# Performance work log

Measured on AMD Instinct MI355X. Metric: run time of the kernel, lower is better.

The kernel has to match this reference:

```python
import jax, jax.numpy as jnp
import numpy as np

S = 4096
DMODEL = 1024
DK = 128

def setup_inputs() -> dict:
    key = jax.random.key(0)
    ks = jax.random.split(key, 7)
    X = jax.random.normal(ks[0], (S, DMODEL), dtype=jnp.float32)
    # nn.Linear(dmodel, dk): weight [dk, dmodel], bias [dk]
    sc = 1.0 / np.sqrt(DMODEL)
    Wq = jax.random.uniform(ks[1], (DK, DMODEL), jnp.float32, -sc, sc)
    bq = jax.random.uniform(ks[2], (DK,), jnp.float32, -sc, sc)
    Wk = jax.random.uniform(ks[3], (DK, DMODEL), jnp.float32, -sc, sc)
    bk = jax.random.uniform(ks[4], (DK,), jnp.float32, -sc, sc)
    Wv = jax.random.uniform(ks[5], (DK, DMODEL), jnp.float32, -sc, sc)
    bv = jax.random.uniform(ks[6], (DK,), jnp.float32, -sc, sc)
    return {"X": X, "Wq": Wq, "bq": bq, "Wk": Wk, "bk": bk, "Wv": Wv, "bv": bv}

def reference(X, Wq, bq, Wk, bk, Wv, bv):
    # QKV projections: [S, dk]
    Q = X @ Wq.T + bq
    K = X @ Wk.T + bk
    V = X @ Wv.T + bv
    scale = 1.0 / jnp.sqrt(jnp.asarray(DK, X.dtype))
    scores = (Q @ K.T) * scale  # [S, S]
    s = X.shape[0]
    causal = jnp.tril(jnp.ones((s, s), dtype=bool))  # True = keep
    scores = jnp.where(causal, scores, -jnp.inf)
    A = jax.nn.softmax(scores, axis=-1)  # dropout p=0 -> identity
    return A @ V  # [S, dk]
```

## Files before the change

### kernel.cpp

```cpp
#include <hip/hip_runtime.h>
#include <hip/hip_bf16.h>

#define S 4096
#define DMODEL 1024
#define DK 128

typedef __attribute__((ext_vector_type(8))) short  short8;
typedef __attribute__((ext_vector_type(4))) float  f32x4;

__device__ __forceinline__ unsigned short f2bf(float f) {
    return __builtin_bit_cast(unsigned short, __float2bfloat16(f));
}

__device__ __forceinline__ short8 cvt8(float4 a, float4 b) {
    short8 v;
    v[0] = (short)f2bf(a.x); v[1] = (short)f2bf(a.y);
    v[2] = (short)f2bf(a.z); v[3] = (short)f2bf(a.w);
    v[4] = (short)f2bf(b.x); v[5] = (short)f2bf(b.y);
    v[6] = (short)f2bf(b.z); v[7] = (short)f2bf(b.w);
    return v;
}

__global__ __launch_bounds__(256) void cvt_kernel(
    const float* __restrict__ X,
    const float* __restrict__ Wq, const float* __restrict__ Wk,
    const float* __restrict__ Wv,
    unsigned short* __restrict__ Xb, unsigned short* __restrict__ Wb)
{
    const int i = blockIdx.x * 256 + threadIdx.x;
    const float* __restrict__ src;
    unsigned short* __restrict__ dst;
    size_t off;
    if (i < 524288) {
        src = X; dst = Xb; off = (size_t)i * 8;
    } else {
        const int j   = i - 524288;
        const int sel = j >> 14, jj = j & 16383;
        src = sel == 0 ? Wq : sel == 1 ? Wk : Wv;
        dst = Wb + (size_t)sel * DK * DMODEL;
        off = (size_t)jj * 8;
    }
    const float4 a = *(const float4*)(src + off);
    const float4 b = *(const float4*)(src + off + 4);
    *(short8*)(dst + off) = cvt8(a, b);
}

__global__ __launch_bounds__(128) void proj_gemm(
    const unsigned short* __restrict__ Xb, const unsigned short* __restrict__ Wb,
    const float* __restrict__ bq, const float* __restrict__ bk,
    const float* __restrict__ bv,
    unsigned short* __restrict__ Qb, unsigned short* __restrict__ Kb,
    unsigned short* __restrict__ Vb)
{
    const int sel = blockIdx.y;
    const float* __restrict__ bias = sel == 0 ? bq : sel == 1 ? bk : bv;
    unsigned short* __restrict__ Out = sel == 0 ? Qb : sel == 1 ? Kb : Vb;
    const unsigned short* __restrict__ wbase = Wb + (size_t)sel * DK * DMODEL;

    const int tid = threadIdx.x, w = tid >> 6, lane = tid & 63;
    const int li = lane & 15, gl = lane >> 4;
    const int r0 = blockIdx.x * 16;
    const int n0 = w * 64;

    f32x4 acc[4];
    #pragma unroll
    for (int j = 0; j < 4; ++j)
        #pragma unroll
        for (int r = 0; r < 4; ++r) acc[j][r] = 0.f;

    const unsigned short* ap = &Xb[(size_t)(r0 + li) * DMODEL + 8 * gl];
    const unsigned short* bp0 = &wbase[(size_t)(n0 + li) * DMODEL + 8 * gl];
    const unsigned short* bp1 = bp0 + (size_t)16 * DMODEL;
    const unsigned short* bp2 = bp0 + (size_t)32 * DMODEL;
    const unsigned short* bp3 = bp0 + (size_t)48 * DMODEL;

    #pragma unroll 4
    for (int k0 = 0; k0 < DMODEL; k0 += 32) {
        const short8 a  = *(const short8*)(ap + k0);
        const short8 b0 = *(const short8*)(bp0 + k0);
        const short8 b1 = *(const short8*)(bp1 + k0);
        const short8 b2 = *(const short8*)(bp2 + k0);
        const short8 b3 = *(const short8*)(bp3 + k0);
        acc[0] = __builtin_amdgcn_mfma_f32_16x16x32_bf16(a, b0, acc[0], 0, 0, 0);
        acc[1] = __builtin_amdgcn_mfma_f32_16x16x32_bf16(a, b1, acc[1], 0, 0, 0);
        acc[2] = __builtin_amdgcn_mfma_f32_16x16x32_bf16(a, b2, acc[2], 0, 0, 0);
        acc[3] = __builtin_amdgcn_mfma_f32_16x16x32_bf16(a, b3, acc[3], 0, 0, 0);
    }

    #pragma unroll
    for (int j = 0; j < 4; ++j)
        #pragma unroll
        for (int r = 0; r < 4; ++r) {
            const int row = r0 + 4 * gl + r;
            const int col = n0 + 16 * j + li;
            Out[(size_t)row * DK + col] = f2bf(acc[j][r] + bias[col]);
        }
}

__global__ __launch_bounds__(256) void transpose_v(
    const unsigned short* __restrict__ Vb, unsigned short* __restrict__ Vt)
{
    __shared__ unsigned short tile[64][72];
    const int s0 = blockIdx.x * 64, d0 = blockIdx.y * 64;
    const int t = threadIdx.x;
    const int r = t >> 2, cc = (t & 3) * 16;

    const short8* src = (const short8*)&Vb[(size_t)(s0 + r) * DK + d0 + cc];
    const short8 a = src[0], b = src[1];
    #pragma unroll
    for (int i = 0; i < 8; ++i) {
        tile[r][cc + i]     = (unsigned short)a[i];
        tile[r][cc + 8 + i] = (unsigned short)b[i];
    }
    __syncthreads();

    short8 o0, o1;
    #pragma unroll
    for (int i = 0; i < 8; ++i) {
        o0[i] = (short)tile[cc + i][r];
        o1[i] = (short)tile[cc + 8 + i][r];
    }
    short8* dst = (short8*)&Vt[(size_t)(d0 + r) * S + s0 + cc];
    dst[0] = o0; dst[1] = o1;
}

__global__ __launch_bounds__(64) void attn_mfma(
    const unsigned short* __restrict__ Qb,
    const unsigned short* __restrict__ Kb,
    const unsigned short* __restrict__ Vt,
    float* __restrict__ OP, float* __restrict__ ML)
{
    const int b = blockIdx.x;
    int g = 0;
    while (4 * (g + 1) * (g + 2) <= b) ++g;
    const int off = b - 4 * g * (g + 1);
    const int t   = 8 * g + off / (g + 1);
    const int c   = off % (g + 1);
    const int kstart = c * 256;
    const int kend   = min((c + 1) * 256, 32 * t + 32);

    const int lane = threadIdx.x, li = lane & 15, gl = lane >> 4;

    __shared__ unsigned short Pl[32][40];

    short8 aq[2][4];
    #pragma unroll
    for (int qs = 0; qs < 2; ++qs)
        #pragma unroll
        for (int s = 0; s < 4; ++s)
            aq[qs][s] = *(const short8*)
                &Qb[(size_t)(32 * t + 16 * qs + li) * DK + 32 * s + 8 * gl];

    f32x4 accv[2][8];
    #pragma unroll
    for (int qs = 0; qs < 2; ++qs)
        #pragma unroll
        for (int n = 0; n < 8; ++n)
            #pragma unroll
            for (int r = 0; r < 4; ++r) accv[qs][n][r] = 0.f;

    float mrow[2][4], lrow[2][4];
    #pragma unroll
    for (int qs = 0; qs < 2; ++qs)
        #pragma unroll
        for (int r = 0; r < 4; ++r) { mrow[qs][r] = -1e30f; lrow[qs][r] = 0.f; }

    const float scale = 0.08838834764831845f;

    short8 bkc[2][4], bkn[2][4];
    #pragma unroll
    for (int kt = 0; kt < 2; ++kt)
        #pragma unroll
        for (int s = 0; s < 4; ++s)
            bkc[kt][s] = *(const short8*)
                &Kb[(size_t)(kstart + 16 * kt + li) * DK + 32 * s + 8 * gl];

    for (int kb = kstart; kb < kend; kb += 32) {
        short8 bv[8];
        #pragma unroll
        for (int n = 0; n < 8; ++n)
            bv[n] = *(const short8*)&Vt[(size_t)(16 * n + li) * S + kb + 8 * gl];

        f32x4 sc[2][2];
        #pragma unroll
        for (int qs = 0; qs < 2; ++qs)
            #pragma unroll
            for (int kt = 0; kt < 2; ++kt)
                #pragma unroll
                for (int r = 0; r < 4; ++r) sc[qs][kt][r] = 0.f;
        __builtin_amdgcn_s_setprio(1);
        #pragma unroll
        for (int qs = 0; qs < 2; ++qs)
            #pragma unroll
            for (int kt = 0; kt < 2; ++kt)
                #pragma unroll
                for (int s = 0; s < 4; ++s)
                    sc[qs][kt] = __builtin_amdgcn_mfma_f32_16x16x32_bf16(
                        aq[qs][s], bkc[kt][s], sc[qs][kt], 0, 0, 0);
        __builtin_amdgcn_s_setprio(0);

        const int kn = (kb + 32 < kend) ? kb + 32 : kb;
        #pragma unroll
        for (int kt = 0; kt < 2; ++kt)
            #pragma unroll
            for (int s = 0; s < 4; ++s)
                bkn[kt][s] = *(const short8*)
                    &Kb[(size_t)(kn + 16 * kt + li) * DK + 32 * s + 8 * gl];

        #pragma unroll
        for (int qs = 0; qs < 2; ++qs)
            #pragma unroll
            for (int kt = 0; kt < 2; ++kt)
                #pragma unroll
                for (int r = 0; r < 4; ++r) {
                    const int key = kb + 16 * kt + li;
                    const int q   = 32 * t + 16 * qs + 4 * gl + r;
                    sc[qs][kt][r] = (key > q) ? -1e30f : sc[qs][kt][r] * scale;
                }

        float tm[2][4];
        #pragma unroll
        for (int qs = 0; qs < 2; ++qs)
            #pragma unroll
            for (int r = 0; r < 4; ++r) {
                float v = fmaxf(sc[qs][0][r], sc[qs][1][r]);
                v = fmaxf(v, __shfl_xor(v, 1));
                v = fmaxf(v, __shfl_xor(v, 2));
                v = fmaxf(v, __shfl_xor(v, 4));
                v = fmaxf(v, __shfl_xor(v, 8));
                tm[qs][r] = v;
            }

        int need = 0;
        #pragma unroll
        for (int qs = 0; qs < 2; ++qs)
            #pragma unroll
            for (int r = 0; r < 4; ++r)
                need |= (tm[qs][r] > mrow[qs][r] + 6.f) ? 1 : 0;
        if (__any(need)) {
            #pragma unroll
            for (int qs = 0; qs < 2; ++qs)
                #pragma unroll
                for (int r = 0; r < 4; ++r) {
                    const float mnew = fmaxf(mrow[qs][r], tm[qs][r]);
                    const float corr = __expf(mrow[qs][r] - mnew);
                    lrow[qs][r] *= corr;
                    mrow[qs][r] = mnew;
                    #pragma unroll
                    for (int n = 0; n < 8; ++n) accv[qs][n][r] *= corr;
                }
        }

        #pragma unroll
        for (int qs = 0; qs < 2; ++qs)
            #pragma unroll
            for (int r = 0; r < 4; ++r) {
                const float p0 = __expf(sc[qs][0][r] - mrow[qs][r]);
                const float p1 = __expf(sc[qs][1][r] - mrow[qs][r]);
                sc[qs][0][r] = p0; sc[qs][1][r] = p1;
                float ps = p0 + p1;
                ps += __shfl_xor(ps, 1);
                ps += __shfl_xor(ps, 2);
                ps += __shfl_xor(ps, 4);
                ps += __shfl_xor(ps, 8);
                lrow[qs][r] += ps;
            }

        #pragma unroll
        for (int qs = 0; qs < 2; ++qs)
            #pragma unroll
            for (int kt = 0; kt < 2; ++kt)
                #pragma unroll
                for (int r = 0; r < 4; ++r)
                    Pl[16 * qs + 4 * gl + r][16 * kt + li] = f2bf(sc[qs][kt][r]);
        __syncthreads();
        const short8 pa0 = *(const short8*)&Pl[li][8 * gl];
        const short8 pa1 = *(const short8*)&Pl[16 + li][8 * gl];
        __syncthreads();

        __builtin_amdgcn_s_setprio(1);
        #pragma unroll
        for (int n = 0; n < 8; ++n) {
            accv[0][n] = __builtin_amdgcn_mfma_f32_16x16x32_bf16(pa0, bv[n], accv[0][n], 0, 0, 0);
            accv[1][n] = __builtin_amdgcn_mfma_f32_16x16x32_bf16(pa1, bv[n], accv[1][n], 0, 0, 0);
        }
        __builtin_amdgcn_s_setprio(0);

        #pragma unroll
        for (int kt = 0; kt < 2; ++kt)
            #pragma unroll
            for (int s = 0; s < 4; ++s) bkc[kt][s] = bkn[kt][s];
    }

    #pragma unroll
    for (int qs = 0; qs < 2; ++qs)
        #pragma unroll
        for (int n = 0; n < 8; ++n)
            #pragma unroll
            for (int r = 0; r < 4; ++r)
                OP[((size_t)b * 32 + 16 * qs + 4 * gl + r) * DK + 16 * n + li]
                    = accv[qs][n][r];
    if (li == 0) {
        #pragma unroll
        for (int qs = 0; qs < 2; ++qs)
            #pragma unroll
            for (int r = 0; r < 4; ++r) {
                ML[((size_t)b * 32 + 16 * qs + 4 * gl + r) * 2 + 0] = mrow[qs][r];
                ML[((size_t)b * 32 + 16 * qs + 4 * gl + r) * 2 + 1] = lrow[qs][r];
            }
    }
}

__global__ __launch_bounds__(DK) void merge_kernel(
    const float* __restrict__ OP, const float* __restrict__ ML,
    float* __restrict__ out)
{
    const int row = blockIdx.x, dv = threadIdx.x;
    const int t  = row >> 5, rl = row & 31;
    const int g  = t >> 3;
    const int base = 4 * g * (g + 1) + (t & 7) * (g + 1);

    float M = -1e30f;
    for (int c = 0; c <= g; ++c)
        M = fmaxf(M, ML[((size_t)(base + c) * 32 + rl) * 2]);
    float L = 0.f, o = 0.f;
    for (int c = 0; c <= g; ++c) {
        const float mc = ML[((size_t)(base + c) * 32 + rl) * 2 + 0];
        const float lc = ML[((size_t)(base + c) * 32 + rl) * 2 + 1];
        const float wgt = __expf(mc - M);
        L += lc * wgt;
        o += wgt * OP[((size_t)(base + c) * 32 + rl) * DK + dv];
    }
    out[(size_t)row * DK + dv] = o / L;
}

extern "C" void kernel_launch(void* const* d_in, const int* in_sizes, int n_in,
                              void* d_out, int out_size, void* d_ws, size_t ws_size,
                              hipStream_t stream)
{
    (void)in_sizes; (void)n_in; (void)out_size; (void)ws_size;
    const float* X  = (const float*)d_in[0];
    const float* Wq = (const float*)d_in[1];
    const float* bq = (const float*)d_in[2];
    const float* Wk = (const float*)d_in[3];
    const float* bk = (const float*)d_in[4];
    const float* Wv = (const float*)d_in[5];
    const float* bv = (const float*)d_in[6];
    float* out = (float*)d_out;

    unsigned short* Wb = (unsigned short*)d_ws;
    unsigned short* Qb = Wb + (size_t)3 * DK * DMODEL;
    unsigned short* Kb = Qb + (size_t)S * DK;
    unsigned short* Vb = Kb + (size_t)S * DK;
    unsigned short* Vt = Vb + (size_t)S * DK;
    unsigned short* Xb = Vt + (size_t)S * DK;
    float* OP = (float*)Xb;
    float* ML = OP + (size_t)1088 * 32 * DK;

    cvt_kernel<<<2240, 256, 0, stream>>>(X, Wq, Wk, Wv, Xb, Wb);
    proj_gemm<<<dim3(S / 16, 3), 128, 0, stream>>>(
        Xb, Wb, bq, bk, bv, Qb, Kb, Vb);
    transpose_v<<<dim3(S / 64, DK / 64), 256, 0, stream>>>(Vb, Vt);
    attn_mfma<<<1088, 64, 0, stream>>>(Qb, Kb, Vt, OP, ML);
    merge_kernel<<<S, DK, 0, stream>>>(OP, ML, out);
}
```

Baseline: 149.9 us.

## Fuse V transpose into projection, split-K finer, swap MFMA operands for per-lane softmax

The projection GEMM now writes V directly in transposed layout, so the separate transpose kernel goes away. Attention work is split into 128-key chunks instead of 256, giving 2112 blocks, and the blocks are launched in reverse order so the largest ones start first. The score MFMA has its operands swapped so each lane owns one query row, which reduces the softmax max/sum reductions to two cross-lane shuffles and lets P be written to LDS as vectors. The __syncthreads calls around the single-wave LDS exchange are removed. The finer split produces more partial results for the merge kernel to combine and write out.

After: 152.3 us. Within noise of the previous version (+1.6%).

```diff
diff --git a/kernel.cpp b/kernel.cpp
--- a/kernel.cpp
+++ b/kernel.cpp
@@ -4,9 +4,11 @@
 #define S 4096
 #define DMODEL 1024
 #define DK 128
+#define NB_ATTN 2112
 
 typedef __attribute__((ext_vector_type(8))) short  short8;
 typedef __attribute__((ext_vector_type(4))) float  f32x4;
+typedef __attribute__((ext_vector_type(4))) unsigned short u16x4;
 
 __device__ __forceinline__ unsigned short f2bf(float f) {
     return __builtin_bit_cast(unsigned short, __float2bfloat16(f));
@@ -50,11 +52,10 @@
     const float* __restrict__ bq, const float* __restrict__ bk,
     const float* __restrict__ bv,
     unsigned short* __restrict__ Qb, unsigned short* __restrict__ Kb,
-    unsigned short* __restrict__ Vb)
+    unsigned short* __restrict__ Vt)
 {
     const int sel = blockIdx.y;
     const float* __restrict__ bias = sel == 0 ? bq : sel == 1 ? bk : bv;
-    unsigned short* __restrict__ Out = sel == 0 ? Qb : sel == 1 ? Kb : Vb;
     const unsigned short* __restrict__ wbase = Wb + (size_t)sel * DK * DMODEL;
 
     const int tid = threadIdx.x, w = tid >> 6, lane = tid & 63;
@@ -68,7 +69,7 @@
         #pragma unroll
         for (int r = 0; r < 4; ++r) acc[j][r] = 0.f;
 
-    const unsigned short* ap = &Xb[(size_t)(r0 + li) * DMODEL + 8 * gl];
+    const unsigned short* ap  = &Xb[(size_t)(r0 + li) * DMODEL + 8 * gl];
     const unsigned short* bp0 = &wbase[(size_t)(n0 + li) * DMODEL + 8 * gl];
     const unsigned short* bp1 = bp0 + (size_t)16 * DMODEL;
     const unsigned short* bp2 = bp0 + (size_t)32 * DMODEL;
@@ -87,41 +88,27 @@
         acc[3] = __builtin_amdgcn_mfma_f32_16x16x32_bf16(a, b3, acc[3], 0, 0, 0);
     }
 
-    #pragma unroll
-    for (int j = 0; j < 4; ++j)
-        #pragma unroll
-        for (int r = 0; r < 4; ++r) {
-            const int row = r0 + 4 * gl + r;
+    if (sel < 2) {
+        unsigned short* __restrict__ Out = sel == 0 ? Qb : Kb;
+        #pragma unroll
+        for (int j = 0; j < 4; ++j)
+            #pragma unroll
+            for (int r = 0; r < 4; ++r) {
+                const int row = r0 + 4 * gl + r;
+                const int col = n0 + 16 * j + li;
+                Out[(size_t)row * DK + col] = f2bf(acc[j][r] + bias[col]);
+            }
+    } else {
+        #pragma unroll
+        for (int j = 0; j < 4; ++j) {
             const int col = n0 + 16 * j + li;
-            Out[(size_t)row * DK + col] = f2bf(acc[j][r] + bias[col]);
-        }
-}
-
-__global__ __launch_bounds__(256) void transpose_v(
-    const unsigned short* __restrict__ Vb, unsigned short* __restrict__ Vt)
-{
-    __shared__ unsigned short tile[64][72];
-    const int s0 = blockIdx.x * 64, d0 = blockIdx.y * 64;
-    const int t = threadIdx.x;
-    const int r = t >> 2, cc = (t & 3) * 16;
-
-    const short8* src = (const short8*)&Vb[(size_t)(s0 + r) * DK + d0 + cc];
-    const short8 a = src[0], b = src[1];
-    #pragma unroll
-    for (int i = 0; i < 8; ++i) {
-        tile[r][cc + i]     = (unsigned short)a[i];
-        tile[r][cc + 8 + i] = (unsigned short)b[i];
-    }
-    __syncthreads();
-
-    short8 o0, o1;
-    #pragma unroll
-    for (int i = 0; i < 8; ++i) {
-        o0[i] = (short)tile[cc + i][r];
-        o1[i] = (short)tile[cc + 8 + i][r];
-    }
-    short8* dst = (short8*)&Vt[(size_t)(d0 + r) * S + s0 + cc];
-    dst[0] = o0; dst[1] = o1;
+            const float bb = bias[col];
+            u16x4 wv;
+            #pragma unroll
+            for (int r = 0; r < 4; ++r) wv[r] = f2bf(acc[j][r] + bb);
+            *(u16x4*)&Vt[(size_t)col * S + r0 + 4 * gl] = wv;
+        }
+    }
 }
 
 __global__ __launch_bounds__(64) void attn_mfma(
@@ -130,14 +117,14 @@
     const unsigned short* __restrict__ Vt,
     float* __restrict__ OP, float* __restrict__ ML)
 {
-    const int b = blockIdx.x;
-    int g = 0;
-    while (4 * (g + 1) * (g + 2) <= b) ++g;
-    const int off = b - 4 * g * (g + 1);
-    const int t   = 8 * g + off / (g + 1);
-    const int c   = off % (g + 1);
-    const int kstart = c * 256;
-    const int kend   = min((c + 1) * 256, 32 * t + 32);
+    const int b = (NB_ATTN - 1) - (int)blockIdx.x;
+    int j = 1;
+    while (2 * (j + 1) * j <= b) ++j;
+    const int off = b - 2 * j * (j - 1);
+    const int t   = 4 * (j - 1) + off / j;
+    const int c   = off % j;
+    const int kstart = 128 * c;
+    const int kend   = min(128 * (c + 1), 32 * t + 32);
 
     const int lane = threadIdx.x, li = lane & 15, gl = lane >> 4;
 
@@ -159,12 +146,7 @@
             #pragma unroll
             for (int r = 0; r < 4; ++r) accv[qs][n][r] = 0.f;
 
-    float mrow[2][4], lrow[2][4];
-    #pragma unroll
-    for (int qs = 0; qs < 2; ++qs)
-        #pragma unroll
-        for (int r = 0; r < 4; ++r) { mrow[qs][r] = -1e30f; lrow[qs][r] = 0.f; }
-
+    float mr[2] = {-1e30f, -1e30f}, lr[2] = {0.f, 0.f};
     const float scale = 0.08838834764831845f;
 
     short8 bkc[2][4], bkn[2][4];
@@ -196,7 +178,7 @@
                 #pragma unroll
                 for (int s = 0; s < 4; ++s)
                     sc[qs][kt] = __builtin_amdgcn_mfma_f32_16x16x32_bf16(
-                        aq[qs][s], bkc[kt][s], sc[qs][kt], 0, 0, 0);
+                        bkc[kt][s], aq[qs][s], sc[qs][kt], 0, 0, 0);
         __builtin_amdgcn_s_setprio(0);
 
         const int kn = (kb + 32 < kend) ? kb + 32 : kb;
@@ -208,75 +190,76 @@
                     &Kb[(size_t)(kn + 16 * kt + li) * DK + 32 * s + 8 * gl];
 
         #pragma unroll
-        for (int qs = 0; qs < 2; ++qs)
+        for (int qs = 0; qs < 2; ++qs) {
+            const int q = 32 * t + 16 * qs + li;
             #pragma unroll
             for (int kt = 0; kt < 2; ++kt)
                 #pragma unroll
                 for (int r = 0; r < 4; ++r) {
-                    const int key = kb + 16 * kt + li;
-                    const int q   = 32 * t + 16 * qs + 4 * gl + r;
+                    const int key = kb + 16 * kt + 4 * gl + r;
                     sc[qs][kt][r] = (key > q) ? -1e30f : sc[qs][kt][r] * scale;
                 }
-
-        float tm[2][4];
+        }
+
+        float tm[2];
+        #pragma unroll
+        for (int qs = 0; qs < 2; ++qs) {
+            float v = fmaxf(fmaxf(fmaxf(sc[qs][0][0], sc[qs][0][1]),
+                                  fmaxf(sc[qs][0][2], sc[qs][0][3])),
+                            fmaxf(fmaxf(sc[qs][1][0], sc[qs][1][1]),
+                                  fmaxf(sc[qs][1][2], sc[qs][1][3])));
+            v = fmaxf(v, __shfl_xor(v, 16));
+            v = fmaxf(v, __shfl_xor(v, 32));
+            tm[qs] = v;
+        }
+
+        const int need = (tm[0] > mr[0] + 6.f) | (tm[1] > mr[1] + 6.f);
+        if (__any(need)) {
+            float corr[2];
+            #pragma unroll
+            for (int qs = 0; qs < 2; ++qs) {
+                const float mnew = fmaxf(mr[qs], tm[qs]);
+                corr[qs] = __expf(mr[qs] - mnew);
+                lr[qs] *= corr[qs];
+                mr[qs]  = mnew;
+            }
+            #pragma unroll
+            for (int qs = 0; qs < 2; ++qs)
+                #pragma unroll
+                for (int r = 0; r < 4; ++r) {
+                    const float cr = __shfl(corr[qs], 4 * gl + r);
+                    #pragma unroll
+                    for (int n = 0; n < 8; ++n) accv[qs][n][r] *= cr;
+                }
+        }
+
+        #pragma unroll
+        for (int qs = 0; qs < 2; ++qs) {
+            float ps = 0.f;
+            #pragma unroll
+            for (int kt = 0; kt < 2; ++kt)
+                #pragma unroll
+                for (int r = 0; r < 4; ++r) {
+                    const float p = __expf(sc[qs][kt][r] - mr[qs]);
+                    sc[qs][kt][r] = p;
+                    ps += p;
+                }
+            ps += __shfl_xor(ps, 16);
+            ps += __shfl_xor(ps, 32);
+            lr[qs] += ps;
+        }
+
         #pragma unroll
         for (int qs = 0; qs < 2; ++qs)
             #pragma unroll
-            for (int r = 0; r < 4; ++r) {
-                float v = fmaxf(sc[qs][0][r], sc[qs][1][r]);
-                v = fmaxf(v, __shfl_xor(v, 1));
-                v = fmaxf(v, __shfl_xor(v, 2));
-                v = fmaxf(v, __shfl_xor(v, 4));
-                v = fmaxf(v, __shfl_xor(v, 8));
-                tm[qs][r] = v;
+            for (int kt = 0; kt < 2; ++kt) {
+                u16x4 wv;
+                #pragma unroll
+                for (int r = 0; r < 4; ++r) wv[r] = f2bf(sc[qs][kt][r]);
+                *(u16x4*)&Pl[16 * qs + li][16 * kt + 4 * gl] = wv;
             }
-
-        int need = 0;
-        #pragma unroll
-        for (int qs = 0; qs < 2; ++qs)
-            #pragma unroll
-            for (int r = 0; r < 4; ++r)
-                need |= (tm[qs][r] > mrow[qs][r] + 6.f) ? 1 : 0;
-        if (__any(need)) {
-            #pragma unroll
-            for (int qs = 0; qs < 2; ++qs)
-                #pragma unroll
-                for (int r = 0; r < 4; ++r) {
-                    const float mnew = fmaxf(mrow[qs][r], tm[qs][r]);
-                    const float corr = __expf(mrow[qs][r] - mnew);
-                    lrow[qs][r] *= corr;
-                    mrow[qs][r] = mnew;
-                    #pragma unroll
-                    for (int n = 0; n < 8; ++n) accv[qs][n][r] *= corr;
-                }
-        }
-
-        #pragma unroll
-        for (int qs = 0; qs < 2; ++qs)
-            #pragma unroll
-            for (int r = 0; r < 4; ++r) {
-                const float p0 = __expf(sc[qs][0][r] - mrow[qs][r]);
-                const float p1 = __expf(sc[qs][1][r] - mrow[qs][r]);
-                sc[qs][0][r] = p0; sc[qs][1][r] = p1;
-                float ps = p0 + p1;
-                ps += __shfl_xor(ps, 1);
-                ps += __shfl_xor(ps, 2);
-                ps += __shfl_xor(ps, 4);
-                ps += __shfl_xor(ps, 8);
-                lrow[qs][r] += ps;
-            }
-
-        #pragma unroll
-        for (int qs = 0; qs < 2; ++qs)
-            #pragma unroll
-            for (int kt = 0; kt < 2; ++kt)
-                #pragma unroll
-                for (int r = 0; r < 4; ++r)
-                    Pl[16 * qs + 4 * gl + r][16 * kt + li] = f2bf(sc[qs][kt][r]);
-        __syncthreads();
         const short8 pa0 = *(const short8*)&Pl[li][8 * gl];
         const short8 pa1 = *(const short8*)&Pl[16 + li][8 * gl];
-        __syncthreads();
 
         __builtin_amdgcn_s_setprio(1);
         #pragma unroll
@@ -300,14 +283,12 @@
             for (int r = 0; r < 4; ++r)
                 OP[((size_t)b * 32 + 16 * qs + 4 * gl + r) * DK + 16 * n + li]
                     = accv[qs][n][r];
-    if (li == 0) {
-        #pragma unroll
-        for (int qs = 0; qs < 2; ++qs)
-            #pragma unroll
-            for (int r = 0; r < 4; ++r) {
-                ML[((size_t)b * 32 + 16 * qs + 4 * gl + r) * 2 + 0] = mrow[qs][r];
-                ML[((size_t)b * 32 + 16 * qs + 4 * gl + r) * 2 + 1] = lrow[qs][r];
-            }
+    if (gl == 0) {
+        #pragma unroll
+        for (int qs = 0; qs < 2; ++qs) {
+            ML[((size_t)b * 32 + 16 * qs + li) * 2 + 0] = mr[qs];
+            ML[((size_t)b * 32 + 16 * qs + li) * 2 + 1] = lr[qs];
+        }
     }
 }
 
@@ -317,14 +298,14 @@
 {
     const int row = blockIdx.x, dv = threadIdx.x;
     const int t  = row >> 5, rl = row & 31;
-    const int g  = t >> 3;
-    const int base = 4 * g * (g + 1) + (t & 7) * (g + 1);
+    const int j  = (t >> 2) + 1;
+    const int base = 2 * j * (j - 1) + (t & 3) * j;
 
     float M = -1e30f;
-    for (int c = 0; c <= g; ++c)
+    for (int c = 0; c < j; ++c)
         M = fmaxf(M, ML[((size_t)(base + c) * 32 + rl) * 2]);
     float L = 0.f, o = 0.f;
-    for (int c = 0; c <= g; ++c) {
+    for (int c = 0; c < j; ++c) {
         const float mc = ML[((size_t)(base + c) * 32 + rl) * 2 + 0];
         const float lc = ML[((size_t)(base + c) * 32 + rl) * 2 + 1];
         const float wgt = __expf(mc - M);
@@ -351,16 +332,14 @@
     unsigned short* Wb = (unsigned short*)d_ws;
     unsigned short* Qb = Wb + (size_t)3 * DK * DMODEL;
     unsigned short* Kb = Qb + (size_t)S * DK;
-    unsigned short* Vb = Kb + (size_t)S * DK;
-    unsigned short* Vt = Vb + (size_t)S * DK;
+    unsigned short* Vt = Kb + (size_t)S * DK;
     unsigned short* Xb = Vt + (size_t)S * DK;
     float* OP = (float*)Xb;
-    float* ML = OP + (size_t)1088 * 32 * DK;
+    float* ML = OP + (size_t)NB_ATTN * 32 * DK;
 
     cvt_kernel<<<2240, 256, 0, stream>>>(X, Wq, Wk, Wv, Xb, Wb);
     proj_gemm<<<dim3(S / 16, 3), 128, 0, stream>>>(
-        Xb, Wb, bq, bk, bv, Qb, Kb, Vb);
-    transpose_v<<<dim3(S / 64, DK / 64), 256, 0, stream>>>(Vb, Vt);
-    attn_mfma<<<1088, 64, 0, stream>>>(Qb, Kb, Vt, OP, ML);
+        Xb, Wb, bq, bk, bv, Qb, Kb, Vt);
+    attn_mfma<<<NB_ATTN, 64, 0, stream>>>(Qb, Kb, Vt, OP, ML);
     merge_kernel<<<S, DK, 0, stream>>>(OP, ML, out);
 }
```
